# Kernel tuning notes

Hardware: AMD Instinct MI355X
Metric: run time of the kernel (lower is better)

The kernel has to match this reference:

```python
import jax, jax.numpy as jnp
import numpy as np
import math

S, B, D = 2048, 8, 256
HEADS = 8
DPROJ = 128
DFF = 1024
DH = DPROJ // HEADS  # 16


def _layernorm(x, g, b, eps=1e-5):
    mu = jnp.mean(x, axis=-1, keepdims=True)
    var = jnp.mean((x - mu) ** 2, axis=-1, keepdims=True)
    return (x - mu) * jax.lax.rsqrt(var + eps) * g + b


def setup_inputs() -> dict:
    key = jax.random.key(0)
    ks = jax.random.split(key, 16)
    s = 0.02
    return {
        "src": jax.random.normal(ks[0], (S, B, D), dtype=jnp.float32),
        "Wq": jax.random.normal(ks[1], (D, DPROJ), dtype=jnp.float32) * s,
        "bq": jnp.zeros((DPROJ,), dtype=jnp.float32),
        "Wk": jax.random.normal(ks[2], (D, DPROJ), dtype=jnp.float32) * s,
        "bk": jnp.zeros((DPROJ,), dtype=jnp.float32),
        "Wv": jax.random.normal(ks[3], (D, DPROJ), dtype=jnp.float32) * s,
        "bv": jnp.zeros((DPROJ,), dtype=jnp.float32),
        "Wo": jax.random.normal(ks[4], (DPROJ, D), dtype=jnp.float32) * s,
        "ln1_g": jnp.ones((D,), dtype=jnp.float32),
        "ln1_b": jnp.zeros((D,), dtype=jnp.float32),
        "W1": jax.random.normal(ks[5], (D, DFF), dtype=jnp.float32) * s,
        "b1": jnp.zeros((DFF,), dtype=jnp.float32),
        "W2": jax.random.normal(ks[6], (DFF, D), dtype=jnp.float32) * s,
        "b2": jnp.zeros((D,), dtype=jnp.float32),
        "ln2_g": jnp.ones((D,), dtype=jnp.float32),
        "ln2_b": jnp.zeros((D,), dtype=jnp.float32),
    }


def reference(src, Wq, bq, Wk, bk, Wv, bv, Wo, ln1_g, ln1_b, W1, b1, W2, b2, ln2_g, ln2_b):
    # src: (S, B, D)
    q = src @ Wq + bq  # (S, B, DPROJ)
    k = src @ Wk + bk
    v = src @ Wv + bv

    # _reshape_to_batches: (S, B, h*dh) -> (S, B*h, dh), then sdpa moves batch first
    def split_heads(x):
        return jnp.transpose(x.reshape(S, B * HEADS, DH), (1, 0, 2))  # (B*h, S, dh)

    qh, kh, vh = split_heads(q), split_heads(k), split_heads(v)
    scores = jnp.einsum('bid,bjd->bij', qh, kh) / math.sqrt(DH)  # (B*h, S, S)
    attn = jax.nn.softmax(scores, axis=-1)
    ctx = jnp.einsum('bij,bjd->bid', attn, vh)  # (B*h, S, dh)

    # _reshape_from_batches: (B*h, S, dh) -> (S, B, DPROJ)
    ctx = jnp.transpose(ctx, (1, 0, 2)).reshape(S, B, DPROJ)
    y = ctx @ Wo  # (S, B, D), no bias

    x = _layernorm(src + y, ln1_g, ln1_b)
    ffn = jax.nn.relu(x @ W1 + b1) @ W2 + b2
    return _layernorm(x + ffn, ln2_g, ln2_b)
```

## Files before the change

kernel.cpp:

```cpp
#include <hip/hip_runtime.h>
#include <math.h>

#define SLEN 2048
#define BATCH 8
#define DMODEL 256
#define HEADS 8
#define DPROJ 128
#define DFF 1024
#define DH 16
#define MROWS (SLEN*BATCH)

typedef unsigned short u16;
typedef unsigned int u32;
typedef __attribute__((ext_vector_type(8))) short short8;
typedef __attribute__((ext_vector_type(4))) float f32x4;
typedef __attribute__((ext_vector_type(4))) unsigned short u16x4;

__device__ __forceinline__ u16 f2bf(float x) {
    union { float f; u32 u; } v; v.f = x;
    u32 r = v.u + 0x7FFFu + ((v.u >> 16) & 1u);
    return (u16)(r >> 16);
}
__device__ __forceinline__ float bf2f(u16 h) {
    union { u32 u; float f; } v; v.u = ((u32)h) << 16;
    return v.f;
}
__device__ __forceinline__ float fexp2(float x) { return __builtin_amdgcn_exp2f(x); }
__device__ __forceinline__ u32 pack_bf(float lo, float hi) {
    union { float f; u32 u; } a, b; a.f = lo; b.f = hi;
    return __builtin_amdgcn_perm(b.u, a.u, 0x07060302u);
}
__device__ __forceinline__ void gld16(const u16* g, u16* l) {
    __builtin_amdgcn_global_load_lds(
        (const __attribute__((address_space(1))) void*)g,
        (__attribute__((address_space(3))) void*)l, 16, 0, 0);
}

__global__ void prep_kernel(const float* __restrict__ src, u16* __restrict__ srcb,
                            const float* __restrict__ Wq, const float* __restrict__ Wk,
                            const float* __restrict__ Wv, const float* __restrict__ Wo,
                            const float* __restrict__ W1, const float* __restrict__ W2,
                            u16* __restrict__ WqT, u16* __restrict__ WkT,
                            u16* __restrict__ WvT, u16* __restrict__ WoT,
                            u16* __restrict__ W1T, u16* __restrict__ W2T) {
    if (blockIdx.x < 4096) {
        int idx = (blockIdx.x * 256 + threadIdx.x) * 4;
        float4 v = *(const float4*)(src + idx);
        u16x4 o;
        o.x = f2bf(v.x); o.y = f2bf(v.y); o.z = f2bf(v.z); o.w = f2bf(v.w);
        *(u16x4*)(srcb + idx) = o;
        return;
    }
    int i = (blockIdx.x - 4096) * 256 + threadIdx.x;
    if (i < 32768) {
        int n = i >> 8, k = i & 255;
        WqT[i] = f2bf(Wq[k * 128 + n]);
    } else if (i < 65536) {
        int j = i - 32768; int n = j >> 8, k = j & 255;
        WkT[j] = f2bf(Wk[k * 128 + n]);
    } else if (i < 98304) {
        int j = i - 65536; int n = j >> 8, k = j & 255;
        WvT[j] = f2bf(Wv[k * 128 + n]);
    } else if (i < 131072) {
        int j = i - 98304; int n = j >> 7, k = j & 127;
        WoT[j] = f2bf(Wo[k * 256 + n]);
    } else if (i < 393216) {
        int j = i - 131072; int n = j >> 8, k = j & 255;
        W1T[j] = f2bf(W1[k * 1024 + n]);
    } else if (i < 655360) {
        int j = i - 393216; int n = j >> 10, k = j & 1023;
        W2T[j] = f2bf(W2[k * 256 + n]);
    }
}

template<int BN, bool RELU, bool HAS_BIAS, bool OUT_BF16>
__global__ void mfma_gemm(const u16* __restrict__ A, const u16* __restrict__ BT,
                          const float* __restrict__ bias, void* __restrict__ Cout,
                          int M, int N, int K) {
    constexpr int NJ = BN / 32;
    __shared__ __align__(16) u16 As[128 * 32];
    __shared__ __align__(16) u16 Bs[BN * 32];
    const int tid = threadIdx.x;
    const int row0 = blockIdx.x * 128;
    const int col0 = blockIdx.y * BN;
    const int w = tid >> 6, l = tid & 63;
    const int wr = (w & 1) * 64, wc = (w >> 1) * (BN / 2);
    const int lcol = l & 15, lrow = (l >> 4) * 4, g = l >> 4;
    const int sl = l >> 2;
    const int swc = ((l & 3) ^ (sl & 3)) * 8;
    const int fsw = (g ^ (lcol & 3)) * 8;

    const u16* Ag0 = A + (size_t)(row0 + 16 * w + sl) * K + swc;
    const u16* Ag1 = Ag0 + (size_t)64 * K;
    const u16* Bg0 = BT + (size_t)(col0 + 16 * w + sl) * K + swc;
    const u16* Bg1 = Bg0 + (size_t)64 * K;
    u16* lA0 = As + (16 * w) * 32;
    u16* lA1 = As + (16 * w + 64) * 32;
    u16* lB0 = Bs + (16 * w) * 32;
    u16* lB1 = Bs + (16 * w + 64) * 32;

    f32x4 acc[4][NJ] = {};
    for (int k0 = 0; k0 < K; k0 += 32) {
        gld16(Ag0 + k0, lA0);
        gld16(Ag1 + k0, lA1);
        gld16(Bg0 + k0, lB0);
        if (BN == 128) gld16(Bg1 + k0, lB1);
        __syncthreads();
        short8 af[4], bf[NJ];
        #pragma unroll
        for (int i = 0; i < 4; ++i)
            af[i] = *(const short8*)(As + (wr + i * 16 + lcol) * 32 + fsw);
        #pragma unroll
        for (int j = 0; j < NJ; ++j)
            bf[j] = *(const short8*)(Bs + (wc + j * 16 + lcol) * 32 + fsw);
        #pragma unroll
        for (int i = 0; i < 4; ++i)
            #pragma unroll
            for (int j = 0; j < NJ; ++j)
                acc[i][j] = __builtin_amdgcn_mfma_f32_16x16x32_bf16(
                    af[i], bf[j], acc[i][j], 0, 0, 0);
        __syncthreads();
    }
    float bv[NJ];
    #pragma unroll
    for (int j = 0; j < NJ; ++j)
        bv[j] = HAS_BIAS ? bias[col0 + wc + j * 16 + lcol] : 0.f;
    #pragma unroll
    for (int i = 0; i < 4; ++i) {
        #pragma unroll
        for (int r = 0; r < 4; ++r) {
            size_t grow = row0 + wr + i * 16 + lrow + r;
            #pragma unroll
            for (int j = 0; j < NJ; ++j) {
                int gcol = col0 + wc + j * 16 + lcol;
                float c = acc[i][j][r] + bv[j];
                if (RELU) c = fmaxf(c, 0.f);
                if (OUT_BF16) ((u16*)Cout)[grow * N + gcol] = f2bf(c);
                else          ((float*)Cout)[grow * N + gcol] = c;
            }
        }
    }
}

__global__ void qkv_mfma(const u16* __restrict__ A,
                         const u16* __restrict__ WqT, const u16* __restrict__ WkT,
                         const u16* __restrict__ WvT,
                         const float* __restrict__ bq, const float* __restrict__ bk,
                         const float* __restrict__ bv,
                         u16* __restrict__ qhp, u16* __restrict__ khp,
                         u16* __restrict__ vhb) {
    const int which = blockIdx.z;
    const u16* BT   = which == 0 ? WqT : (which == 1 ? WkT : WvT);
    const float* bs = which == 0 ? bq : (which == 1 ? bk : bv);
    const float scale = which == 0 ? 0.25f * 1.44269504f : 1.0f;
    __shared__ __align__(16) u16 As[128 * 32];
    __shared__ __align__(16) u16 Bs[128 * 32];
    const int tid = threadIdx.x;
    const int row0 = blockIdx.x * 128;
    const int w = tid >> 6, l = tid & 63;
    const int wr = (w & 1) * 64, wc = (w >> 1) * 64;
    const int lcol = l & 15, lrow = (l >> 4) * 4, g = l >> 4;
    const int sl = l >> 2;
    const int swc = ((l & 3) ^ (sl & 3)) * 8;
    const int fsw = (g ^ (lcol & 3)) * 8;

    const u16* Ag0 = A + (size_t)(row0 + 16 * w + sl) * DMODEL + swc;
    const u16* Ag1 = Ag0 + (size_t)64 * DMODEL;
    const u16* Bg0 = BT + (size_t)(16 * w + sl) * DMODEL + swc;
    const u16* Bg1 = Bg0 + (size_t)64 * DMODEL;
    u16* lA0 = As + (16 * w) * 32;
    u16* lA1 = As + (16 * w + 64) * 32;
    u16* lB0 = Bs + (16 * w) * 32;
    u16* lB1 = Bs + (16 * w + 64) * 32;

    f32x4 acc[4][4] = {};
    for (int k0 = 0; k0 < DMODEL; k0 += 32) {
        gld16(Ag0 + k0, lA0);
        gld16(Ag1 + k0, lA1);
        gld16(Bg0 + k0, lB0);
        gld16(Bg1 + k0, lB1);
        __syncthreads();
        short8 af[4], bf[4];
        #pragma unroll
        for (int i = 0; i < 4; ++i)
            af[i] = *(const short8*)(As + (wr + i * 16 + lcol) * 32 + fsw);
        #pragma unroll
        for (int j = 0; j < 4; ++j)
            bf[j] = *(const short8*)(Bs + (wc + j * 16 + lcol) * 32 + fsw);
        #pragma unroll
        for (int i = 0; i < 4; ++i)
            #pragma unroll
            for (int j = 0; j < 4; ++j)
                acc[i][j] = __builtin_amdgcn_mfma_f32_16x16x32_bf16(
                    af[i], bf[j], acc[i][j], 0, 0, 0);
        __syncthreads();
    }
    #pragma unroll
    for (int i = 0; i < 4; ++i) {
        #pragma unroll
        for (int r = 0; r < 4; ++r) {
            int grow = row0 + wr + i * 16 + lrow + r;
            int b = grow & 7, s = grow >> 3;
            #pragma unroll
            for (int j = 0; j < 4; ++j) {
                int gcol = wc + j * 16 + lcol;
                int h = gcol >> 4, d = gcol & 15;
                float c = acc[i][j][r] + bs[gcol];
                if (which == 2) {
                    vhb[((size_t)(b * 8 + h) * SLEN + s) * 16 + d] = f2bf(c);
                } else {
                    u16* base = (which == 0 ? qhp : khp)
                              + ((size_t)(b * 8 + h) * SLEN + s) * 32;
                    base[d] = f2bf(c * scale);
                    base[d + 16] = 0;
                }
            }
        }
    }
}

__global__ void transpose_v(const u16* __restrict__ vhb, u16* __restrict__ vT) {
    __shared__ u16 T[128 * 24];
    const int bh = blockIdx.y;
    const int c0 = blockIdx.x * 128;
    const int t = threadIdx.x;
    {
        int key = t >> 1, half = t & 1;
        *(uint4*)(T + key * 24 + half * 8) =
            *(const uint4*)(vhb + ((size_t)bh * SLEN + c0 + key) * 16 + half * 8);
    }
    __syncthreads();
    int d = t >> 4, k8 = (t & 15) * 8;
    u16x4 o0, o1;
    o0.x = T[(k8 + 0) * 24 + d]; o0.y = T[(k8 + 1) * 24 + d];
    o0.z = T[(k8 + 2) * 24 + d]; o0.w = T[(k8 + 3) * 24 + d];
    o1.x = T[(k8 + 4) * 24 + d]; o1.y = T[(k8 + 5) * 24 + d];
    o1.z = T[(k8 + 6) * 24 + d]; o1.w = T[(k8 + 7) * 24 + d];
    u16* dst = vT + ((size_t)bh * 16 + d) * SLEN + c0 + k8;
    *(u16x4*)dst = o0;
    *(u16x4*)(dst + 4) = o1;
}

__global__ __launch_bounds__(256, 8)
void attn_mfma(const u16* __restrict__ qg, const u16* __restrict__ kg,
               const u16* __restrict__ vT, u16* __restrict__ ctx) {
    __shared__ __align__(16) u16 Ps[4 * 32 * 76];
    const int bh = blockIdx.y;
    const int q0 = blockIdx.x * 64;
    const int tid = threadIdx.x;
    const int w = tid >> 6, l = tid & 63;
    const int qw = w & 1;
    const int z  = w >> 1;
    const int qc = l & 15, g = l >> 4;
    u16* Pw = Ps + w * 2432;

    short8 qf[2];
    {
        const u16* qbase = qg + ((size_t)bh * SLEN + q0 + qw * 32) * 32;
        qf[0] = *(const short8*)(qbase + qc * 32 + 8 * g);
        qf[1] = *(const short8*)(qbase + (16 + qc) * 32 + 8 * g);
    }
    const u16* kbase = kg + (size_t)bh * SLEN * 32;
    const u16* vbase = vT + ((size_t)bh * 16 + qc) * SLEN;

    f32x4 o_[2] = {};
    f32x4 ls[2] = {};
    const short one_bf = (short)0x3F80;
    short8 onesB = {one_bf, one_bf, one_bf, one_bf, one_bf, one_bf, one_bf, one_bf};

    for (int t = 0; t < 16; ++t) {
        const int k0 = (z * 16 + t) * 64;
        short8 kf[4], vf[2];
        #pragma unroll
        for (int kj = 0; kj < 4; ++kj)
            kf[kj] = *(const short8*)(kbase + (size_t)(k0 + kj * 16 + qc) * 32 + 8 * g);
        #pragma unroll
        for (int ks = 0; ks < 2; ++ks)
            vf[ks] = *(const short8*)(vbase + k0 + ks * 32 + 8 * g);

        f32x4 s_[4][2];
        #pragma unroll
        for (int kj = 0; kj < 4; ++kj)
            #pragma unroll
            for (int mi = 0; mi < 2; ++mi) {
                f32x4 zz = {0.f, 0.f, 0.f, 0.f};
                s_[kj][mi] = __builtin_amdgcn_mfma_f32_16x16x32_bf16(
                    kf[kj], qf[mi], zz, 0, 0, 0);
            }
        #pragma unroll
        for (int mi = 0; mi < 2; ++mi)
            #pragma unroll
            for (int kj = 0; kj < 4; ++kj) {
                f32x4 sv = s_[kj][mi];
                uint2 dd;
                dd.x = pack_bf(fexp2(sv[0]), fexp2(sv[1]));
                dd.y = pack_bf(fexp2(sv[2]), fexp2(sv[3]));
                *(uint2*)(Pw + (mi * 16 + qc) * 76 + kj * 16 + 4 * g) = dd;
            }
        #pragma unroll
        for (int ks = 0; ks < 2; ++ks) {
            #pragma unroll
            for (int mi = 0; mi < 2; ++mi) {
                const u16* rp = Pw + (mi * 16 + qc) * 76 + ks * 32 + 8 * g;
                union { uint2 q[2]; short8 v; } ap;
                ap.q[0] = *(const uint2*)rp;
                ap.q[1] = *(const uint2*)(rp + 4);
                o_[mi] = __builtin_amdgcn_mfma_f32_16x16x32_bf16(ap.v, vf[ks], o_[mi], 0, 0, 0);
                ls[mi] = __builtin_amdgcn_mfma_f32_16x16x32_bf16(ap.v, onesB, ls[mi], 0, 0, 0);
            }
        }
    }

    __syncthreads();
    float* Ms = (float*)Ps;
    const int base = qw * 64 + l;
    if (z == 1) {
        #pragma unroll
        for (int k = 0; k < 4; ++k) {
            Ms[(k     ) * 128 + base] = o_[0][k];
            Ms[(k +  4) * 128 + base] = o_[1][k];
            Ms[(k +  8) * 128 + base] = ls[0][k];
            Ms[(k + 12) * 128 + base] = ls[1][k];
        }
    }
    __syncthreads();
    if (z == 0) {
        #pragma unroll
        for (int k = 0; k < 4; ++k) {
            o_[0][k] += Ms[(k     ) * 128 + base];
            o_[1][k] += Ms[(k +  4) * 128 + base];
            ls[0][k] += Ms[(k +  8) * 128 + base];
            ls[1][k] += Ms[(k + 12) * 128 + base];
        }
        const int b = bh >> 3, h = bh & 7;
        #pragma unroll
        for (int mi = 0; mi < 2; ++mi)
            #pragma unroll
            for (int r = 0; r < 4; ++r) {
                int qrow = q0 + qw * 32 + mi * 16 + 4 * g + r;
                ctx[((size_t)qrow * BATCH + b) * DPROJ + h * DH + qc] =
                    f2bf(o_[mi][r] / ls[mi][r]);
            }
    }
}

__global__ void ln1_kernel(const float* __restrict__ src, const u16* __restrict__ y,
                           const float* __restrict__ g, const float* __restrict__ bb,
                           u16* __restrict__ xb) {
    const int w = threadIdx.x >> 6, l = threadIdx.x & 63;
    const int row = blockIdx.x * 4 + w;
    const int c = l * 4;
    size_t base = (size_t)row * DMODEL;
    float4 s4 = *(const float4*)(src + base + c);
    u16x4 y4 = *(const u16x4*)(y + base + c);
    float v[4] = { s4.x + bf2f(y4.x), s4.y + bf2f(y4.y),
                   s4.z + bf2f(y4.z), s4.w + bf2f(y4.w) };
    float sum = v[0] + v[1] + v[2] + v[3];
    float ss  = v[0]*v[0] + v[1]*v[1] + v[2]*v[2] + v[3]*v[3];
    #pragma unroll
    for (int off = 1; off < 64; off <<= 1) {
        sum += __shfl_xor(sum, off);
        ss  += __shfl_xor(ss, off);
    }
    float mu = sum * (1.0f / 256.0f);
    float var = ss * (1.0f / 256.0f) - mu * mu;
    float rs = rsqrtf(var + 1e-5f);
    float4 g4 = *(const float4*)(g + c);
    float4 b4 = *(const float4*)(bb + c);
    u16x4 o;
    o.x = f2bf((v[0] - mu) * rs * g4.x + b4.x);
    o.y = f2bf((v[1] - mu) * rs * g4.y + b4.y);
    o.z = f2bf((v[2] - mu) * rs * g4.z + b4.z);
    o.w = f2bf((v[3] - mu) * rs * g4.w + b4.w);
    *(u16x4*)(xb + base + c) = o;
}

__global__ void ln2_kernel(const u16* __restrict__ x, const u16* __restrict__ f,
                           const float* __restrict__ g, const float* __restrict__ bb,
                           float* __restrict__ out) {
    const int w = threadIdx.x >> 6, l = threadIdx.x & 63;
    const int row = blockIdx.x * 4 + w;
    const int c = l * 4;
    size_t base = (size_t)row * DMODEL;
    u16x4 x4 = *(const u16x4*)(x + base + c);
    u16x4 f4 = *(const u16x4*)(f + base + c);
    float v[4] = { bf2f(x4.x) + bf2f(f4.x), bf2f(x4.y) + bf2f(f4.y),
                   bf2f(x4.z) + bf2f(f4.z), bf2f(x4.w) + bf2f(f4.w) };
    float sum = v[0] + v[1] + v[2] + v[3];
    float ss  = v[0]*v[0] + v[1]*v[1] + v[2]*v[2] + v[3]*v[3];
    #pragma unroll
    for (int off = 1; off < 64; off <<= 1) {
        sum += __shfl_xor(sum, off);
        ss  += __shfl_xor(ss, off);
    }
    float mu = sum * (1.0f / 256.0f);
    float var = ss * (1.0f / 256.0f) - mu * mu;
    float rs = rsqrtf(var + 1e-5f);
    float4 g4 = *(const float4*)(g + c);
    float4 b4 = *(const float4*)(bb + c);
    float4 o;
    o.x = (v[0] - mu) * rs * g4.x + b4.x;
    o.y = (v[1] - mu) * rs * g4.y + b4.y;
    o.z = (v[2] - mu) * rs * g4.z + b4.z;
    o.w = (v[3] - mu) * rs * g4.w + b4.w;
    *(float4*)(out + base + c) = o;
}

extern "C" void kernel_launch(void* const* d_in, const int* in_sizes, int n_in,
                              void* d_out, int out_size, void* d_ws, size_t ws_size,
                              hipStream_t stream) {
    const float* src = (const float*)d_in[0];
    const float* Wq  = (const float*)d_in[1];
    const float* bq  = (const float*)d_in[2];
    const float* Wk  = (const float*)d_in[3];
    const float* bk  = (const float*)d_in[4];
    const float* Wv  = (const float*)d_in[5];
    const float* bv  = (const float*)d_in[6];
    const float* Wo  = (const float*)d_in[7];
    const float* g1  = (const float*)d_in[8];
    const float* be1 = (const float*)d_in[9];
    const float* W1  = (const float*)d_in[10];
    const float* b1  = (const float*)d_in[11];
    const float* W2  = (const float*)d_in[12];
    const float* b2  = (const float*)d_in[13];
    const float* g2  = (const float*)d_in[14];
    const float* be2 = (const float*)d_in[15];
    char* ws = (char*)d_ws;
    float* out = (float*)d_out;

    u16* qhp  = (u16*)(ws + 0);
    u16* khp  = (u16*)(ws + 8388608);
    u16* vhb  = (u16*)(ws + 16777216);
    u16* vT   = (u16*)(ws + 20971520);
    u16* ctxb = (u16*)(ws + 25165824);
    u16* yb   = (u16*)(ws + 29360128);
    u16* hb   = (u16*)(ws + 0);
    u16* xb   = (u16*)(ws + 37748736);
    u16* fb   = (u16*)(ws + 46137344);
    u16* srcb = (u16*)(ws + 54525952);
    u16* WqT  = (u16*)(ws + 62914560);
    u16* WkT  = (u16*)(ws + 62980096);
    u16* WvT  = (u16*)(ws + 63045632);
    u16* WoT  = (u16*)(ws + 63111168);
    u16* W1T  = (u16*)(ws + 63176704);
    u16* W2T  = (u16*)(ws + 63700992);

    prep_kernel<<<6656, 256, 0, stream>>>(src, srcb, Wq, Wk, Wv, Wo, W1, W2,
                                          WqT, WkT, WvT, WoT, W1T, W2T);
    qkv_mfma<<<dim3(128, 1, 3), 256, 0, stream>>>(srcb, WqT, WkT, WvT,
                                                  bq, bk, bv, qhp, khp, vhb);
    transpose_v<<<dim3(16, 64), 256, 0, stream>>>(vhb, vT);
    attn_mfma<<<dim3(32, 64), 256, 0, stream>>>(qhp, khp, vT, ctxb);
    mfma_gemm<64, false, false, true><<<dim3(128, 4), 256, 0, stream>>>(
        ctxb, WoT, nullptr, yb, MROWS, DMODEL, DPROJ);
    ln1_kernel<<<MROWS / 4, 256, 0, stream>>>(src, yb, g1, be1, xb);
    mfma_gemm<128, true, true, true><<<dim3(128, 8), 256, 0, stream>>>(
        xb, W1T, b1, hb, MROWS, DFF, DMODEL);
    mfma_gemm<64, false, true, true><<<dim3(128, 4), 256, 0, stream>>>(
        hb, W2T, b2, fb, MROWS, DMODEL, DFF);
    ln2_kernel<<<MROWS / 4, 256, 0, stream>>>(xb, fb, g2, be2, out);
}
```

Baseline: 232.4 us.

## Double-buffer K/V tiles in LDS and keep P in registers for attention

The attention kernel now stages K and V^T tiles into swizzled, double-buffered shared memory with async global-to-LDS loads, prefetching the next tile while computing the current one. It no longer round-trips the softmax P matrix through LDS and instead packs it directly into MFMA A-operand registers, using a permuted V fragment layout to match. The aim is to hide global-load latency and remove the LDS write/read of P. In exchange it adds a per-iteration block barrier, uses more LDS, and lowers the occupancy hint from 8 to 4 waves per SIMD.

After: 214.8 us. 1.08x faster.

```diff
diff --git a/kernel.cpp b/kernel.cpp
--- a/kernel.cpp
+++ b/kernel.cpp
@@ -241,10 +241,11 @@
     *(u16x4*)(dst + 4) = o1;
 }
 
-__global__ __launch_bounds__(256, 8)
+__global__ __launch_bounds__(256, 4)
 void attn_mfma(const u16* __restrict__ qg, const u16* __restrict__ kg,
                const u16* __restrict__ vT, u16* __restrict__ ctx) {
-    __shared__ __align__(16) u16 Ps[4 * 32 * 76];
+    __shared__ __align__(16) u16 Ks[2][2][64 * 32];
+    __shared__ __align__(16) u16 Vs[2][2][16 * 64];
     const int bh = blockIdx.y;
     const int q0 = blockIdx.x * 64;
     const int tid = threadIdx.x;
@@ -252,7 +253,6 @@
     const int qw = w & 1;
     const int z  = w >> 1;
     const int qc = l & 15, g = l >> 4;
-    u16* Pw = Ps + w * 2432;
 
     short8 qf[2];
     {
@@ -260,23 +260,56 @@
         qf[0] = *(const short8*)(qbase + qc * 32 + 8 * g);
         qf[1] = *(const short8*)(qbase + (16 + qc) * 32 + 8 * g);
     }
-    const u16* kbase = kg + (size_t)bh * SLEN * 32;
-    const u16* vbase = vT + ((size_t)bh * 16 + qc) * SLEN;
+
+    const int sl = l >> 2;
+    const int swc = ((l & 3) ^ (sl & 3)) * 8;
+    const size_t kb = (size_t)bh * SLEN * 32 + (size_t)z * 1024 * 32;
+    const u16* Kg0 = kg + kb + (size_t)(32 * qw + sl) * 32 + swc;
+    const u16* Kg1 = kg + kb + (size_t)(32 * qw + 16 + sl) * 32 + swc;
+    u16* lK = (u16*)Ks + z * 2048 + (32 * qw) * 32;
+    const int vr = l >> 3, vc = l & 7;
+    const int vsw = (vc ^ ((8 * qw + vr) & 7)) * 8;
+    const u16* Vg = vT + ((size_t)bh * 16 + 8 * qw + vr) * SLEN
+                       + (size_t)z * 1024 + vsw;
+    u16* lV = (u16*)Vs + z * 1024 + (8 * qw) * 64;
+    const int fsw = (g ^ (qc & 3)) * 8;
+    const int qx = qc & 7, gh = g >> 1, gs = (g & 1) * 4;
+    const int vrow = qc * 64;
 
     f32x4 o_[2] = {};
     f32x4 ls[2] = {};
     const short one_bf = (short)0x3F80;
     short8 onesB = {one_bf, one_bf, one_bf, one_bf, one_bf, one_bf, one_bf, one_bf};
 
+    gld16(Kg0, lK);
+    gld16(Kg1, lK + 16 * 32);
+    gld16(Vg, lV);
+    __syncthreads();
+
+    int cur = 0;
     for (int t = 0; t < 16; ++t) {
-        const int k0 = (z * 16 + t) * 64;
-        short8 kf[4], vf[2];
+        if (t + 1 < 16) {
+            const size_t ko = (size_t)(t + 1) * 64 * 32;
+            const int nb = (cur ^ 1);
+            gld16(Kg0 + ko, lK + nb * 4096);
+            gld16(Kg1 + ko, lK + nb * 4096 + 16 * 32);
+            gld16(Vg + (t + 1) * 64, lV + nb * 2048);
+        }
+        const u16* Kc = (const u16*)Ks + cur * 4096 + z * 2048;
+        const u16* Vc = (const u16*)Vs + cur * 2048 + z * 1024;
+        short8 kf[4];
         #pragma unroll
         for (int kj = 0; kj < 4; ++kj)
-            kf[kj] = *(const short8*)(kbase + (size_t)(k0 + kj * 16 + qc) * 32 + 8 * g);
-        #pragma unroll
-        for (int ks = 0; ks < 2; ++ks)
-            vf[ks] = *(const short8*)(vbase + k0 + ks * 32 + 8 * g);
+            kf[kj] = *(const short8*)(Kc + (kj * 16 + qc) * 32 + fsw);
+        short8 vfrag[2];
+        #pragma unroll
+        for (int ks = 0; ks < 2; ++ks) {
+            union { u32 d[4]; short8 v; } vv;
+            uint2 va = *(const uint2*)(Vc + vrow + ((4 * ks + gh) ^ qx) * 8 + gs);
+            uint2 vb = *(const uint2*)(Vc + vrow + ((4 * ks + 2 + gh) ^ qx) * 8 + gs);
+            vv.d[0] = va.x; vv.d[1] = va.y; vv.d[2] = vb.x; vv.d[3] = vb.y;
+            vfrag[ks] = vv.v;
+        }
 
         f32x4 s_[4][2];
         #pragma unroll
@@ -287,32 +320,30 @@
                 s_[kj][mi] = __builtin_amdgcn_mfma_f32_16x16x32_bf16(
                     kf[kj], qf[mi], zz, 0, 0, 0);
             }
+        u32 dd[2][4][2];
         #pragma unroll
         for (int mi = 0; mi < 2; ++mi)
             #pragma unroll
             for (int kj = 0; kj < 4; ++kj) {
                 f32x4 sv = s_[kj][mi];
-                uint2 dd;
-                dd.x = pack_bf(fexp2(sv[0]), fexp2(sv[1]));
-                dd.y = pack_bf(fexp2(sv[2]), fexp2(sv[3]));
-                *(uint2*)(Pw + (mi * 16 + qc) * 76 + kj * 16 + 4 * g) = dd;
-            }
-        #pragma unroll
-        for (int ks = 0; ks < 2; ++ks) {
+                dd[mi][kj][0] = pack_bf(fexp2(sv[0]), fexp2(sv[1]));
+                dd[mi][kj][1] = pack_bf(fexp2(sv[2]), fexp2(sv[3]));
+            }
+        #pragma unroll
+        for (int ks = 0; ks < 2; ++ks)
             #pragma unroll
             for (int mi = 0; mi < 2; ++mi) {
-                const u16* rp = Pw + (mi * 16 + qc) * 76 + ks * 32 + 8 * g;
-                union { uint2 q[2]; short8 v; } ap;
-                ap.q[0] = *(const uint2*)rp;
-                ap.q[1] = *(const uint2*)(rp + 4);
-                o_[mi] = __builtin_amdgcn_mfma_f32_16x16x32_bf16(ap.v, vf[ks], o_[mi], 0, 0, 0);
+                union { u32 d[4]; short8 v; } ap;
+                ap.d[0] = dd[mi][2 * ks][0];     ap.d[1] = dd[mi][2 * ks][1];
+                ap.d[2] = dd[mi][2 * ks + 1][0]; ap.d[3] = dd[mi][2 * ks + 1][1];
+                o_[mi] = __builtin_amdgcn_mfma_f32_16x16x32_bf16(ap.v, vfrag[ks], o_[mi], 0, 0, 0);
                 ls[mi] = __builtin_amdgcn_mfma_f32_16x16x32_bf16(ap.v, onesB, ls[mi], 0, 0, 0);
             }
-        }
-    }
-
-    __syncthreads();
-    float* Ms = (float*)Ps;
+        __syncthreads();
+        cur ^= 1;
+    }
+
+    float* Ms = (float*)Ks;
     const int base = qw * 64 + l;
     if (z == 1) {
         #pragma unroll
```
